# Performance work log

Measured on AMD Instinct MI355X. Metric: run time of the kernel, lower is better.

Reference implementation:

```python
import jax, jax.numpy as jnp
import numpy as np

N_NODES = 50000
N_EDGES = 800000
N_REL = 16
D = 64          # entity_dim == relation_dim == n_hidden
NEG_SLOPE = 0.01  # torch F.leaky_relu default


def setup_inputs() -> dict:
    key = jax.random.key(0)
    ks = jax.random.split(key, 12)
    s = 1.0 / np.sqrt(D)
    return {
        "node_ids": jnp.arange(N_NODES, dtype=jnp.int64) if jax.config.jax_enable_x64 else jnp.arange(N_NODES, dtype=jnp.int32),
        "relation_ids": jax.random.randint(ks[0], (N_EDGES,), 0, N_REL),
        "src": jax.random.randint(ks[1], (N_EDGES,), 0, N_NODES),
        "dst": jax.random.randint(ks[2], (N_EDGES,), 0, N_NODES),
        "entity_embed": jax.random.normal(ks[3], (N_NODES, D), jnp.float32) * s,
        "relation_embed": jax.random.normal(ks[4], (N_REL, D), jnp.float32) * s,
        "W0": jax.random.normal(ks[5], (N_REL, D, D), jnp.float32) * s,
        "W1": jax.random.normal(ks[6], (N_REL, D, D), jnp.float32) * s,
        "ra0": jax.random.normal(ks[7], (D, D), jnp.float32) * s,
        "rb0": jax.random.normal(ks[8], (D, D), jnp.float32) * s,
        "ra1": jax.random.normal(ks[9], (D, D), jnp.float32) * s,
        "rb1": jax.random.normal(ks[10], (D, D), jnp.float32) * s,
    }


def _edge_softmax(scores, dst, n_nodes):
    # segment softmax over edges grouped by destination node (DGL edge_softmax)
    m = jax.ops.segment_max(scores, dst, num_segments=n_nodes)  # [N]
    e = jnp.exp(scores - m[dst])                                # [E]
    z = jax.ops.segment_sum(e, dst, num_segments=n_nodes)       # [N]
    return e / z[dst]


def _kgat_layer(h, efeat, src, dst, etype, Wr, ra, rb, n_nodes):
    # transform every node under every relation once: [N, R, Dr]
    trans = jnp.einsum('nd,rde->nre', h, Wr)
    t_r = trans[src, etype]                   # W_r h_t  [E, Dr]
    h_r = trans[dst, etype]                   # W_r h_h  [E, Dr]
    att = jnp.sum(t_r * jnp.tanh(h_r + efeat), axis=1)  # [E]
    a = _edge_softmax(att, dst, n_nodes)                 # [E]
    # u_mul_e + sum: scatter-add weighted source features to dst
    h_nb = jax.ops.segment_sum(h[src] * a[:, None], dst, num_segments=n_nodes)
    # Bi residual
    out = (jax.nn.leaky_relu((h + h_nb) @ ra, NEG_SLOPE)
           + jax.nn.leaky_relu((h * h_nb) @ rb, NEG_SLOPE))
    return out


def reference(node_ids, relation_ids, src, dst, entity_embed, relation_embed,
              W0, W1, ra0, rb0, ra1, rb1):
    h = entity_embed[node_ids]                 # [N, D]
    efeat = relation_embed[relation_ids]       # [E, D]
    n_nodes = node_ids.shape[0]
    cache = [h]
    for Wr, ra, rb in ((W0, ra0, rb0), (W1, ra1, rb1)):
        h = _kgat_layer(h, efeat, src, dst, relation_ids, Wr, ra, rb, n_nodes)
        cache.append(h)
    return jnp.concatenate(cache, axis=1)      # [N, 3*D]
```

## Files before the change

### kernel.cpp

```cpp
#include <hip/hip_runtime.h>
#include <hip/hip_bf16.h>
#include <math.h>

#define NN 50000
#define NE 800000
#define NR 16
#define DD 64
#define OSTRIDE 192
#define QSTRIDE 1032

typedef _Float16 f16;
typedef f16 f16x8 __attribute__((ext_vector_type(8)));
typedef f16 f16x2 __attribute__((ext_vector_type(2)));
typedef __attribute__((ext_vector_type(4))) float f32x4;

__device__ inline float tanh_fast(float x) {
    return 1.f - 2.f / (__expf(2.f * x) + 1.f);
}

__device__ inline float dot2acc(f16x2 a, f16x2 b, float c) {
#if __has_builtin(__builtin_amdgcn_fdot2)
    return __builtin_amdgcn_fdot2(a, b, c, false);
#else
    return c + (float)a[0] * (float)b[0] + (float)a[1] * (float)b[1];
#endif
}

#if __has_builtin(__builtin_amdgcn_update_dpp)
__device__ inline float xor1_add(float x) {
    return x + __int_as_float(__builtin_amdgcn_update_dpp(
        0, __float_as_int(x), 0xB1, 0xF, 0xF, true));
}
__device__ inline float xor2_add(float x) {
    return x + __int_as_float(__builtin_amdgcn_update_dpp(
        0, __float_as_int(x), 0x4E, 0xF, 0xF, true));
}
__device__ inline float xor8_add(float x) {
    return x + __int_as_float(__builtin_amdgcn_update_dpp(
        0, __float_as_int(x), 0x108, 0xF, 0xF, true));
}
#else
__device__ inline float xor1_add(float x) { return x + __shfl_xor(x, 1, 64); }
__device__ inline float xor2_add(float x) { return x + __shfl_xor(x, 2, 64); }
__device__ inline float xor8_add(float x) { return x + __shfl_xor(x, 8, 64); }
#endif

__global__ void k_deg(const int* __restrict__ dst, int* __restrict__ cnt) {
    for (int e = blockIdx.x * blockDim.x + threadIdx.x; e < NE;
         e += gridDim.x * blockDim.x)
        atomicAdd(&cnt[dst[e]], 1);
}

__global__ __launch_bounds__(256) void k_scan1(const int* __restrict__ cnt,
                                               int* __restrict__ rowptr,
                                               int* __restrict__ bsum) {
    __shared__ int sh[256];
    int b = blockIdx.x, t = threadIdx.x;
    int i = b * 256 + t;
    int v = (i < NN) ? cnt[i] : 0;
    sh[t] = v;
    __syncthreads();
    #pragma unroll
    for (int o = 1; o < 256; o <<= 1) {
        int u = (t >= o) ? sh[t - o] : 0;
        __syncthreads();
        sh[t] += u;
        __syncthreads();
    }
    if (i < NN) rowptr[i] = sh[t] - v;
    if (t == 255) bsum[b] = sh[255];
}

__global__ __launch_bounds__(256) void k_scan2(int* __restrict__ bsum, int nb) {
    __shared__ int sh[256];
    int t = threadIdx.x;
    int v = (t < nb) ? bsum[t] : 0;
    sh[t] = v;
    __syncthreads();
    #pragma unroll
    for (int o = 1; o < 256; o <<= 1) {
        int u = (t >= o) ? sh[t - o] : 0;
        __syncthreads();
        sh[t] += u;
        __syncthreads();
    }
    if (t < nb) bsum[t] = sh[t] - v;
}

__global__ __launch_bounds__(256) void k_scan3(int* __restrict__ rowptr,
                                               const int* __restrict__ bsum,
                                               int* __restrict__ cursor) {
    int b = blockIdx.x, t = threadIdx.x;
    int i = b * 256 + t;
    if (i < NN) {
        int v = rowptr[i] + bsum[b];
        rowptr[i] = v;
        cursor[i] = v;
    }
    if (i == 0) rowptr[NN] = NE;
}

__global__ void k_fill(const int* __restrict__ dst, const int* __restrict__ src,
                       const int* __restrict__ rel, int* __restrict__ cursor,
                       int* __restrict__ epack) {
    for (int e = blockIdx.x * blockDim.x + threadIdx.x; e < NE;
         e += gridDim.x * blockDim.x) {
        int pos = atomicAdd(&cursor[dst[e]], 1);
        epack[pos] = src[e] | (rel[e] << 16);
    }
}

__global__ void k_copy_h0(const int* __restrict__ node_ids,
                          const float* __restrict__ ent,
                          float* __restrict__ out,
                          f16* __restrict__ hf) {
    int i = blockIdx.x * blockDim.x + threadIdx.x;
    if (i >= NN * DD) return;
    int n = i >> 6, d = i & 63;
    float v = ent[(size_t)node_ids[n] * DD + d];
    out[(size_t)n * OSTRIDE + d] = v;
    hf[(size_t)n * DD + d] = (f16)v;
}

__global__ void k_prep(const float* __restrict__ W,
                       const float* __restrict__ ra, const float* __restrict__ rb,
                       f16* __restrict__ wf, f16* __restrict__ wtf,
                       f16* __restrict__ rat, f16* __restrict__ rbt) {
    int i = blockIdx.x * blockDim.x + threadIdx.x;
    if (i < NR * DD * DD) {
        int r = i >> 12, rem = i & 4095, d = rem >> 6, E = rem & 63;
        f16 v = (f16)W[i];
        wf[i] = v;
        wtf[(r << 12) | (E << 6) | d] = v;
    }
    if (i < DD * DD) {
        int d = i >> 6, dp = i & 63;
        rat[dp * 64 + d] = (f16)ra[i];
        rbt[dp * 64 + d] = (f16)rb[i];
    }
}

__global__ __launch_bounds__(1024) void k_fused10(const f16* __restrict__ hfin,
                                                  const f16* __restrict__ wf,
                                                  const f16* __restrict__ wtf,
                                                  const f16* __restrict__ rat,
                                                  const f16* __restrict__ rbt,
                                                  const float* __restrict__ relE,
                                                  const int* __restrict__ rowptr,
                                                  const int* __restrict__ epack,
                                                  float* __restrict__ out,
                                                  int off_in, int off_out,
                                                  f16* __restrict__ hfout) {
    __shared__ __align__(16) f16 q_lds[16 * QSTRIDE];
    __shared__ __align__(16) f16 u_lds[16][16][72];
    int n0 = blockIdx.x * 16;
    int t  = threadIdx.x;
    int w  = t >> 6, l = t & 63;
    int l15 = l & 15, lg = l >> 4;
    int r = w;

    {
        int ar = n0 + l15;
        const f16* ap = hfin + (size_t)ar * DD + lg * 8;
        f16x8 a0 = *(const f16x8*)ap;
        f16x8 a1 = *(const f16x8*)(ap + 32);

        f32x4 acc[4];
        #pragma unroll
        for (int nt = 0; nt < 4; ++nt) acc[nt] = (f32x4){0.f, 0.f, 0.f, 0.f};
        const f16* wtr = wtf + (r << 12);
        #pragma unroll
        for (int nt = 0; nt < 4; ++nt) {
            const f16* bp = wtr + (nt * 16 + l15) * DD + lg * 8;
            f16x8 b0 = *(const f16x8*)bp;
            f16x8 b1 = *(const f16x8*)(bp + 32);
            acc[nt] = __builtin_amdgcn_mfma_f32_16x16x32_f16(a0, b0, acc[nt], 0, 0, 0);
            acc[nt] = __builtin_amdgcn_mfma_f32_16x16x32_f16(a1, b1, acc[nt], 0, 0, 0);
        }

        #pragma unroll
        for (int nt = 0; nt < 4; ++nt) {
            int E = nt * 16 + l15;
            float er = relE[r * DD + E];
            #pragma unroll
            for (int reg = 0; reg < 4; ++reg)
                u_lds[w][lg * 4 + reg][E] = (f16)tanh_fast(acc[nt][reg] + er);
        }
        asm volatile("s_waitcnt lgkmcnt(0)" ::: "memory");

        const f16* up = &u_lds[w][l15][lg * 8];
        f16x8 u0 = *(const f16x8*)up;
        f16x8 u1 = *(const f16x8*)(up + 32);

        f32x4 q4[4];
        #pragma unroll
        for (int nt = 0; nt < 4; ++nt) q4[nt] = (f32x4){0.f, 0.f, 0.f, 0.f};
        const f16* wr = wf + (r << 12);
        #pragma unroll
        for (int nt = 0; nt < 4; ++nt) {
            const f16* bp = wr + (nt * 16 + l15) * DD + lg * 8;
            f16x8 b0 = *(const f16x8*)bp;
            f16x8 b1 = *(const f16x8*)(bp + 32);
            q4[nt] = __builtin_amdgcn_mfma_f32_16x16x32_f16(u0, b0, q4[nt], 0, 0, 0);
            q4[nt] = __builtin_amdgcn_mfma_f32_16x16x32_f16(u1, b1, q4[nt], 0, 0, 0);
        }

        #pragma unroll
        for (int reg = 0; reg < 4; ++reg) {
            f16* qp = q_lds + (lg * 4 + reg) * QSTRIDE + r * 64 + l15;
            #pragma unroll
            for (int nt = 0; nt < 4; ++nt)
                qp[nt * 16] = (f16)q4[nt][reg];
        }
    }
    __syncthreads();

    int n = n0 + w;
    const f16* ql = q_lds + w * QSTRIDE;
    int row0 = rowptr[n], row1 = rowptr[n + 1];
    int deg = row1 - row0;
    int g  = l >> 3;
    int d8 = l & 7;

    float zr = 0.f;
    float a[8] = {};

    int steps = (deg + 7) >> 3;
    for (int k = 0; k < steps; ++k) {
        int idx = row0 + (k << 3) + g;
        bool ok = idx < row1;
        int p = epack[ok ? idx : row0];
        int s = p & 0xffff, rr = p >> 16;
        f16x8 hv = *(const f16x8*)(hfin + ((size_t)s << 6) + (d8 << 3));
        f16x8 qv = *(const f16x8*)(ql + (rr << 6) + (d8 << 3));
        float dp = 0.f;
        #pragma unroll
        for (int j = 0; j < 4; ++j) {
            f16x2 ha = {hv[2 * j], hv[2 * j + 1]};
            f16x2 qa = {qv[2 * j], qv[2 * j + 1]};
            dp = dot2acc(ha, qa, dp);
        }
        dp = xor1_add(dp);
        dp = xor2_add(dp);
        dp += __shfl_xor(dp, 4, 64);
        float wg = ok ? __expf(dp) : 0.f;
        zr += wg;
        #pragma unroll
        for (int j = 0; j < 8; ++j)
            a[j] = fmaf(wg, (float)hv[j], a[j]);
    }

    zr = xor8_add(zr);
    #pragma unroll
    for (int j = 0; j < 8; ++j) a[j] = xor8_add(a[j]);
    #pragma unroll
    for (int o = 16; o < 64; o <<= 1) {
        zr += __shfl_xor(zr, o, 64);
        #pragma unroll
        for (int j = 0; j < 8; ++j)
            a[j] += __shfl_xor(a[j], o, 64);
    }

    if (g == 0) {
        float inv = (deg > 0) ? 1.f / zr : 0.f;
        f16x8 hrow = *(const f16x8*)(hfin + ((size_t)n << 6) + (d8 << 3));
        f16x8 v1v, v2v;
        #pragma unroll
        for (int j = 0; j < 8; ++j) {
            float h = (float)hrow[j];
            float nb = a[j] * inv;
            v1v[j] = (f16)(h + nb);
            v2v[j] = (f16)(h * nb);
        }
        *(f16x8*)(q_lds + w * QSTRIDE + (d8 << 3)) = v1v;
        *(f16x8*)(q_lds + w * QSTRIDE + 256 + (d8 << 3)) = v2v;
    }
    __syncthreads();

    if (w < 4) {
        const f16* v1p = q_lds + (size_t)l15 * QSTRIDE + lg * 8;
        f16x8 a10 = *(const f16x8*)v1p;
        f16x8 a11 = *(const f16x8*)(v1p + 32);
        const f16* v2p = v1p + 256;
        f16x8 a20 = *(const f16x8*)v2p;
        f16x8 a21 = *(const f16x8*)(v2p + 32);

        const f16* bra = rat + (w * 16 + l15) * 64 + lg * 8;
        f16x8 b10 = *(const f16x8*)bra;
        f16x8 b11 = *(const f16x8*)(bra + 32);
        const f16* brb = rbt + (w * 16 + l15) * 64 + lg * 8;
        f16x8 b20 = *(const f16x8*)brb;
        f16x8 b21 = *(const f16x8*)(brb + 32);

        f32x4 o1 = (f32x4){0.f, 0.f, 0.f, 0.f};
        f32x4 o2 = (f32x4){0.f, 0.f, 0.f, 0.f};
        o1 = __builtin_amdgcn_mfma_f32_16x16x32_f16(a10, b10, o1, 0, 0, 0);
        o1 = __builtin_amdgcn_mfma_f32_16x16x32_f16(a11, b11, o1, 0, 0, 0);
        o2 = __builtin_amdgcn_mfma_f32_16x16x32_f16(a20, b20, o2, 0, 0, 0);
        o2 = __builtin_amdgcn_mfma_f32_16x16x32_f16(a21, b21, o2, 0, 0, 0);

        int dp = w * 16 + l15;
        #pragma unroll
        for (int reg = 0; reg < 4; ++reg) {
            int node = n0 + lg * 4 + reg;
            float u1 = o1[reg], u2 = o2[reg];
            u1 = u1 > 0.f ? u1 : 0.01f * u1;
            u2 = u2 > 0.f ? u2 : 0.01f * u2;
            float v = u1 + u2;
            out[(size_t)node * OSTRIDE + off_out + dp] = v;
            hfout[(size_t)node * DD + dp] = (f16)v;
        }
    }
}

extern "C" void kernel_launch(void* const* d_in, const int* in_sizes, int n_in,
                              void* d_out, int out_size, void* d_ws, size_t ws_size,
                              hipStream_t stream) {
    const int*   node_ids = (const int*)d_in[0];
    const int*   rel_ids  = (const int*)d_in[1];
    const int*   src      = (const int*)d_in[2];
    const int*   dst      = (const int*)d_in[3];
    const float* ent      = (const float*)d_in[4];
    const float* relE     = (const float*)d_in[5];
    const float* W[2]  = {(const float*)d_in[6], (const float*)d_in[7]};
    const float* ra[2] = {(const float*)d_in[8], (const float*)d_in[10]};
    const float* rb[2] = {(const float*)d_in[9], (const float*)d_in[11]};
    float* out = (float*)d_out;

    const size_t hf_bytes     = (size_t)NN * DD * sizeof(f16);
    const size_t wf_bytes     = (size_t)NR * DD * DD * sizeof(f16);
    const size_t rt_bytes     = (size_t)DD * DD * sizeof(f16);
    const size_t epack_bytes  = (size_t)NE * sizeof(int);
    const size_t rowptr_bytes = (size_t)(NN + 1) * sizeof(int);
    const size_t cnt_bytes    = (size_t)NN * sizeof(int);
    const int    NB_SCAN      = (NN + 255) / 256;
    const size_t bsum_bytes   = (size_t)256 * sizeof(int);

    char* p = (char*)d_ws;
    f16*   hf     = (f16*)p;   p += hf_bytes;
    f16*   hf2    = (f16*)p;   p += hf_bytes;
    f16*   wf     = (f16*)p;   p += wf_bytes;
    f16*   wtf    = (f16*)p;   p += wf_bytes;
    f16*   rat    = (f16*)p;   p += rt_bytes;
    f16*   rbt    = (f16*)p;   p += rt_bytes;
    int*   epack  = (int*)p;   p += epack_bytes;
    int*   rowptr = (int*)p;   p += rowptr_bytes;
    int*   cnt    = (int*)p;   p += cnt_bytes;
    int*   bsum   = (int*)p;   p += bsum_bytes;
    (void)ws_size;

    hipMemsetAsync(cnt, 0, cnt_bytes, stream);
    k_deg  <<<1024, 256, 0, stream>>>(dst, cnt);
    k_scan1<<<NB_SCAN, 256, 0, stream>>>(cnt, rowptr, bsum);
    k_scan2<<<1, 256, 0, stream>>>(bsum, NB_SCAN);
    k_scan3<<<NB_SCAN, 256, 0, stream>>>(rowptr, bsum, cnt);
    k_fill <<<1024, 256, 0, stream>>>(dst, src, rel_ids, cnt, epack);

    k_copy_h0<<<(NN * DD + 255) / 256, 256, 0, stream>>>(node_ids, ent, out, hf);

    f16* hin  = hf;
    f16* hout = hf2;
    for (int L = 0; L < 2; ++L) {
        int off_in = L * DD;
        int off_out = (L + 1) * DD;

        k_prep  <<<(NR * DD * DD + 255) / 256, 256, 0, stream>>>(W[L], ra[L], rb[L],
                                                                 wf, wtf, rat, rbt);
        k_fused10<<<NN / 16, 1024, 0, stream>>>(hin, wf, wtf, rat, rbt, relE,
                                                rowptr, epack, out,
                                                off_in, off_out, hout);
        f16* tmp = hin; hin = hout; hout = tmp;
    }
}
```

Measured before the change: 376.0 us.

## Sort nodes by degree into a permutation so fused-kernel blocks get balanced work

Adds a degree histogram and counting-sort pass that builds a permutation of nodes grouped by in-degree. The fused layer kernel then processes nodes through this permutation, so the 16 waves in a block handle nodes of similar degree and fewer waves sit idle waiting on the slowest one. The cost is extra preprocessing launches, atomics, and one more indirection per node, and it reads scattered rows of h and output instead of contiguous ones. The correctness of k_scan2 as an exclusive scan over the histogram is assumed.

```diff
diff --git a/kernel.cpp b/kernel.cpp
--- a/kernel.cpp
+++ b/kernel.cpp
@@ -110,6 +110,19 @@
     }
 }
 
+__global__ void k_hist(const int* __restrict__ cnt, int* __restrict__ hist) {
+    int i = blockIdx.x * blockDim.x + threadIdx.x;
+    if (i < NN) atomicAdd(&hist[min(cnt[i], 255)], 1);
+}
+__global__ void k_permfill(const int* __restrict__ cnt, int* __restrict__ histcur,
+                           int* __restrict__ perm) {
+    int i = blockIdx.x * blockDim.x + threadIdx.x;
+    if (i < NN) {
+        int pos = atomicAdd(&histcur[min(cnt[i], 255)], 1);
+        perm[pos] = i;
+    }
+}
+
 __global__ void k_copy_h0(const int* __restrict__ node_ids,
                           const float* __restrict__ ent,
                           float* __restrict__ out,
@@ -140,7 +153,8 @@
     }
 }
 
-__global__ __launch_bounds__(1024) void k_fused10(const f16* __restrict__ hfin,
+__global__ __launch_bounds__(1024) void k_fused11(const int* __restrict__ perm,
+                                                  const f16* __restrict__ hfin,
                                                   const f16* __restrict__ wf,
                                                   const f16* __restrict__ wtf,
                                                   const f16* __restrict__ rat,
@@ -160,7 +174,7 @@
     int r = w;
 
     {
-        int ar = n0 + l15;
+        int ar = perm[n0 + l15];
         const f16* ap = hfin + (size_t)ar * DD + lg * 8;
         f16x8 a0 = *(const f16x8*)ap;
         f16x8 a1 = *(const f16x8*)(ap + 32);
@@ -215,7 +229,7 @@
     }
     __syncthreads();
 
-    int n = n0 + w;
+    int n = perm[n0 + w];
     const f16* ql = q_lds + w * QSTRIDE;
     int row0 = rowptr[n], row1 = rowptr[n + 1];
     int deg = row1 - row0;
@@ -302,7 +316,7 @@
         int dp = w * 16 + l15;
         #pragma unroll
         for (int reg = 0; reg < 4; ++reg) {
-            int node = n0 + lg * 4 + reg;
+            int node = perm[n0 + lg * 4 + reg];
             float u1 = o1[reg], u2 = o2[reg];
             u1 = u1 > 0.f ? u1 : 0.01f * u1;
             u2 = u2 > 0.f ? u2 : 0.01f * u2;
@@ -333,8 +347,10 @@
     const size_t epack_bytes  = (size_t)NE * sizeof(int);
     const size_t rowptr_bytes = (size_t)(NN + 1) * sizeof(int);
     const size_t cnt_bytes    = (size_t)NN * sizeof(int);
+    const size_t perm_bytes   = (size_t)NN * sizeof(int);
     const int    NB_SCAN      = (NN + 255) / 256;
     const size_t bsum_bytes   = (size_t)256 * sizeof(int);
+    const size_t hist_bytes   = (size_t)256 * sizeof(int);
 
     char* p = (char*)d_ws;
     f16*   hf     = (f16*)p;   p += hf_bytes;
@@ -346,15 +362,21 @@
     int*   epack  = (int*)p;   p += epack_bytes;
     int*   rowptr = (int*)p;   p += rowptr_bytes;
     int*   cnt    = (int*)p;   p += cnt_bytes;
+    int*   perm   = (int*)p;   p += perm_bytes;
     int*   bsum   = (int*)p;   p += bsum_bytes;
+    int*   hist   = (int*)p;   p += hist_bytes;
     (void)ws_size;
 
     hipMemsetAsync(cnt, 0, cnt_bytes, stream);
-    k_deg  <<<1024, 256, 0, stream>>>(dst, cnt);
-    k_scan1<<<NB_SCAN, 256, 0, stream>>>(cnt, rowptr, bsum);
-    k_scan2<<<1, 256, 0, stream>>>(bsum, NB_SCAN);
-    k_scan3<<<NB_SCAN, 256, 0, stream>>>(rowptr, bsum, cnt);
-    k_fill <<<1024, 256, 0, stream>>>(dst, src, rel_ids, cnt, epack);
+    hipMemsetAsync(hist, 0, hist_bytes, stream);
+    k_deg     <<<1024, 256, 0, stream>>>(dst, cnt);
+    k_hist    <<<NB_SCAN, 256, 0, stream>>>(cnt, hist);
+    k_scan2   <<<1, 256, 0, stream>>>(hist, 256);
+    k_permfill<<<NB_SCAN, 256, 0, stream>>>(cnt, hist, perm);
+    k_scan1   <<<NB_SCAN, 256, 0, stream>>>(cnt, rowptr, bsum);
+    k_scan2   <<<1, 256, 0, stream>>>(bsum, NB_SCAN);
+    k_scan3   <<<NB_SCAN, 256, 0, stream>>>(rowptr, bsum, cnt);
+    k_fill    <<<1024, 256, 0, stream>>>(dst, src, rel_ids, cnt, epack);
 
     k_copy_h0<<<(NN * DD + 255) / 256, 256, 0, stream>>>(node_ids, ent, out, hf);
 
@@ -366,7 +388,7 @@
 
         k_prep  <<<(NR * DD * DD + 255) / 256, 256, 0, stream>>>(W[L], ra[L], rb[L],
                                                                  wf, wtf, rat, rbt);
-        k_fused10<<<NN / 16, 1024, 0, stream>>>(hin, wf, wtf, rat, rbt, relE,
+        k_fused11<<<NN / 16, 1024, 0, stream>>>(perm, hin, wf, wtf, rat, rbt, relE,
                                                 rowptr, epack, out,
                                                 off_in, off_out, hout);
         f16* tmp = hin; hin = hout; hout = tmp;
```

Result: slower. 631.9 us (+68.0%).

## Split bi-residual output GEMM out of fused aggregation kernel into separate kernel

Applied to the files above, without the earlier changes.

Moves the final bi-residual MFMA stage (the ra/rb projections, leaky relu and output writes) out of the 1024-thread fused aggregation kernel into a new 256-thread kernel. The aggregation kernel now writes h+nb and h*nb as f16 to a global workspace buffer and returns without the second block barrier and the tail where only 4 of 16 waves work. This frees the large block earlier, but adds a global round trip of about 12.8 MB plus an extra launch per layer.

```diff
diff --git a/kernel.cpp b/kernel.cpp
--- a/kernel.cpp
+++ b/kernel.cpp
@@ -140,17 +140,13 @@
     }
 }
 
-__global__ __launch_bounds__(1024) void k_fused10(const f16* __restrict__ hfin,
+__global__ __launch_bounds__(1024) void k_fused12(const f16* __restrict__ hfin,
                                                   const f16* __restrict__ wf,
                                                   const f16* __restrict__ wtf,
-                                                  const f16* __restrict__ rat,
-                                                  const f16* __restrict__ rbt,
                                                   const float* __restrict__ relE,
                                                   const int* __restrict__ rowptr,
                                                   const int* __restrict__ epack,
-                                                  float* __restrict__ out,
-                                                  int off_in, int off_out,
-                                                  f16* __restrict__ hfout) {
+                                                  f16* __restrict__ v12) {
     __shared__ __align__(16) f16 q_lds[16 * QSTRIDE];
     __shared__ __align__(16) f16 u_lds[16][16][72];
     int n0 = blockIdx.x * 16;
@@ -226,12 +222,13 @@
     float a[8] = {};
 
     int steps = (deg + 7) >> 3;
+    const f16* hb = hfin + (d8 << 3);
     for (int k = 0; k < steps; ++k) {
         int idx = row0 + (k << 3) + g;
         bool ok = idx < row1;
         int p = epack[ok ? idx : row0];
-        int s = p & 0xffff, rr = p >> 16;
-        f16x8 hv = *(const f16x8*)(hfin + ((size_t)s << 6) + (d8 << 3));
+        f16x8 hv = *(const f16x8*)(hb + ((size_t)(p & 0xffff) << 6));
+        int rr = p >> 16;
         f16x8 qv = *(const f16x8*)(ql + (rr << 6) + (d8 << 3));
         float dp = 0.f;
         #pragma unroll
@@ -272,44 +269,53 @@
             v1v[j] = (f16)(h + nb);
             v2v[j] = (f16)(h * nb);
         }
-        *(f16x8*)(q_lds + w * QSTRIDE + (d8 << 3)) = v1v;
-        *(f16x8*)(q_lds + w * QSTRIDE + 256 + (d8 << 3)) = v2v;
-    }
-    __syncthreads();
-
-    if (w < 4) {
-        const f16* v1p = q_lds + (size_t)l15 * QSTRIDE + lg * 8;
-        f16x8 a10 = *(const f16x8*)v1p;
-        f16x8 a11 = *(const f16x8*)(v1p + 32);
-        const f16* v2p = v1p + 256;
-        f16x8 a20 = *(const f16x8*)v2p;
-        f16x8 a21 = *(const f16x8*)(v2p + 32);
-
-        const f16* bra = rat + (w * 16 + l15) * 64 + lg * 8;
-        f16x8 b10 = *(const f16x8*)bra;
-        f16x8 b11 = *(const f16x8*)(bra + 32);
-        const f16* brb = rbt + (w * 16 + l15) * 64 + lg * 8;
-        f16x8 b20 = *(const f16x8*)brb;
-        f16x8 b21 = *(const f16x8*)(brb + 32);
-
-        f32x4 o1 = (f32x4){0.f, 0.f, 0.f, 0.f};
-        f32x4 o2 = (f32x4){0.f, 0.f, 0.f, 0.f};
-        o1 = __builtin_amdgcn_mfma_f32_16x16x32_f16(a10, b10, o1, 0, 0, 0);
-        o1 = __builtin_amdgcn_mfma_f32_16x16x32_f16(a11, b11, o1, 0, 0, 0);
-        o2 = __builtin_amdgcn_mfma_f32_16x16x32_f16(a20, b20, o2, 0, 0, 0);
-        o2 = __builtin_amdgcn_mfma_f32_16x16x32_f16(a21, b21, o2, 0, 0, 0);
-
-        int dp = w * 16 + l15;
-        #pragma unroll
-        for (int reg = 0; reg < 4; ++reg) {
-            int node = n0 + lg * 4 + reg;
-            float u1 = o1[reg], u2 = o2[reg];
-            u1 = u1 > 0.f ? u1 : 0.01f * u1;
-            u2 = u2 > 0.f ? u2 : 0.01f * u2;
-            float v = u1 + u2;
-            out[(size_t)node * OSTRIDE + off_out + dp] = v;
-            hfout[(size_t)node * DD + dp] = (f16)v;
-        }
+        f16* vp = v12 + ((size_t)n << 7);
+        *(f16x8*)(vp + (d8 << 3)) = v1v;
+        *(f16x8*)(vp + 64 + (d8 << 3)) = v2v;
+    }
+}
+
+__global__ __launch_bounds__(256) void k_out3(const f16* __restrict__ v12,
+                                              const f16* __restrict__ rat,
+                                              const f16* __restrict__ rbt,
+                                              float* __restrict__ out,
+                                              int off_out,
+                                              f16* __restrict__ hfout) {
+    int n0 = blockIdx.x * 16;
+    int t  = threadIdx.x;
+    int w  = t >> 6, l = t & 63;
+    int l15 = l & 15, lg = l >> 4;
+
+    const f16* vp = v12 + ((size_t)(n0 + l15) << 7) + lg * 8;
+    f16x8 a10 = *(const f16x8*)vp;
+    f16x8 a11 = *(const f16x8*)(vp + 32);
+    f16x8 a20 = *(const f16x8*)(vp + 64);
+    f16x8 a21 = *(const f16x8*)(vp + 96);
+
+    const f16* bra = rat + (w * 16 + l15) * 64 + lg * 8;
+    f16x8 b10 = *(const f16x8*)bra;
+    f16x8 b11 = *(const f16x8*)(bra + 32);
+    const f16* brb = rbt + (w * 16 + l15) * 64 + lg * 8;
+    f16x8 b20 = *(const f16x8*)brb;
+    f16x8 b21 = *(const f16x8*)(brb + 32);
+
+    f32x4 o1 = (f32x4){0.f, 0.f, 0.f, 0.f};
+    f32x4 o2 = (f32x4){0.f, 0.f, 0.f, 0.f};
+    o1 = __builtin_amdgcn_mfma_f32_16x16x32_f16(a10, b10, o1, 0, 0, 0);
+    o1 = __builtin_amdgcn_mfma_f32_16x16x32_f16(a11, b11, o1, 0, 0, 0);
+    o2 = __builtin_amdgcn_mfma_f32_16x16x32_f16(a20, b20, o2, 0, 0, 0);
+    o2 = __builtin_amdgcn_mfma_f32_16x16x32_f16(a21, b21, o2, 0, 0, 0);
+
+    int dp = w * 16 + l15;
+    #pragma unroll
+    for (int reg = 0; reg < 4; ++reg) {
+        int node = n0 + lg * 4 + reg;
+        float u1 = o1[reg], u2 = o2[reg];
+        u1 = u1 > 0.f ? u1 : 0.01f * u1;
+        u2 = u2 > 0.f ? u2 : 0.01f * u2;
+        float v = u1 + u2;
+        out[(size_t)node * OSTRIDE + off_out + dp] = v;
+        hfout[(size_t)node * DD + dp] = (f16)v;
     }
 }
 
@@ -328,6 +334,7 @@
     float* out = (float*)d_out;
 
     const size_t hf_bytes     = (size_t)NN * DD * sizeof(f16);
+    const size_t v12_bytes    = (size_t)NN * 2 * DD * sizeof(f16);
     const size_t wf_bytes     = (size_t)NR * DD * DD * sizeof(f16);
     const size_t rt_bytes     = (size_t)DD * DD * sizeof(f16);
     const size_t epack_bytes  = (size_t)NE * sizeof(int);
@@ -339,6 +346,7 @@
     char* p = (char*)d_ws;
     f16*   hf     = (f16*)p;   p += hf_bytes;
     f16*   hf2    = (f16*)p;   p += hf_bytes;
+    f16*   v12    = (f16*)p;   p += v12_bytes;
     f16*   wf     = (f16*)p;   p += wf_bytes;
     f16*   wtf    = (f16*)p;   p += wf_bytes;
     f16*   rat    = (f16*)p;   p += rt_bytes;
@@ -361,14 +369,13 @@
     f16* hin  = hf;
     f16* hout = hf2;
     for (int L = 0; L < 2; ++L) {
-        int off_in = L * DD;
         int off_out = (L + 1) * DD;
 
-        k_prep  <<<(NR * DD * DD + 255) / 256, 256, 0, stream>>>(W[L], ra[L], rb[L],
-                                                                 wf, wtf, rat, rbt);
-        k_fused10<<<NN / 16, 1024, 0, stream>>>(hin, wf, wtf, rat, rbt, relE,
-                                                rowptr, epack, out,
-                                                off_in, off_out, hout);
+        k_prep   <<<(NR * DD * DD + 255) / 256, 256, 0, stream>>>(W[L], ra[L], rb[L],
+                                                                  wf, wtf, rat, rbt);
+        k_fused12<<<NN / 16, 1024, 0, stream>>>(hin, wf, wtf, relE,
+                                                rowptr, epack, v12);
+        k_out3   <<<NN / 16, 256, 0, stream>>>(v12, rat, rbt, out, off_out, hout);
         f16* tmp = hin; hin = hout; hout = tmp;
     }
 }
```

Result: slower. 404.7 us (+7.6%).
